# Performance work log

Hardware: AMD Instinct MI355X
Metric: run time of the kernel (lower is better)

The kernel has to match this reference:

```python
import jax, jax.numpy as jnp
import numpy as np

NHEAD, TOKEN_DIM, HIDDEN, OUT_DIM = 4, 768, 256, 768
B, L = 16, 1024
EPS = 1e-5
SLOPE = 0.01  # default LeakyReLU negative_slope


def _layernorm(x, g, b):
    mu = jnp.mean(x, axis=-1, keepdims=True)
    var = jnp.var(x, axis=-1, keepdims=True)
    return (x - mu) * jax.lax.rsqrt(var + EPS) * g + b


def setup_inputs() -> dict:
    key = jax.random.key(0)
    ks = jax.random.split(key, 8)
    s = 0.02
    return {
        "token_embedding": jax.random.normal(ks[0], (B, L, TOKEN_DIM), jnp.float32),
        "W_fc": jax.random.normal(ks[1], (NHEAD, TOKEN_DIM, HIDDEN), jnp.float32) * s,
        "b_fc": jnp.zeros((NHEAD, HIDDEN), jnp.float32),
        "ln_g": jnp.ones((NHEAD, HIDDEN), jnp.float32),
        "ln_b": jnp.zeros((NHEAD, HIDDEN), jnp.float32),
        "a_w": jax.random.normal(ks[2], (NHEAD, 2 * HIDDEN), jnp.float32) * s,
        "a_b": jnp.zeros((NHEAD,), jnp.float32),
        "W_cat": jax.random.normal(ks[3], (NHEAD * HIDDEN, OUT_DIM), jnp.float32) * s,
        "b_cat": jnp.zeros((OUT_DIM,), jnp.float32),
        "lnO_g": jnp.ones((OUT_DIM,), jnp.float32),
        "lnO_b": jnp.zeros((OUT_DIM,), jnp.float32),
        "W_fcs": jax.random.normal(ks[4], (3, OUT_DIM, OUT_DIM), jnp.float32) * s,
        "b_fcs": jnp.zeros((3, OUT_DIM), jnp.float32),
    }


def reference(token_embedding, W_fc, b_fc, ln_g, ln_b, a_w, a_b,
              W_cat, b_cat, lnO_g, lnO_b, W_fcs, b_fcs):
    # per-head projection + layernorm: h [n, B, L, H]
    h = jnp.einsum('bld,ndh->nblh', token_embedding, W_fc) + b_fc[:, None, None, :]
    h = _layernorm(h, ln_g[:, None, None, :], ln_b[:, None, None, :])
    # attn_fc(concat[h_j, h_i]) decomposes linearly:
    # score[n,b,i,j] = a1 . h[n,b,j] + a2 . h[n,b,i] + bias
    s_row = jnp.einsum('nblh,nh->nbl', h, a_w[:, :HIDDEN])   # varies with j
    s_col = jnp.einsum('nblh,nh->nbl', h, a_w[:, HIDDEN:])   # varies with i
    e = s_col[:, :, :, None] + s_row[:, :, None, :] + a_b[:, None, None, None]
    e = jnp.where(e >= 0, e, SLOPE * e)  # LeakyReLU
    attn = jax.nn.softmax(e, axis=-1)    # softmax over j
    h_prime = jnp.einsum('nbij,nbjh->nbih', attn, h)  # [n, B, L, H]
    # concat heads on feature dim -> [B, L, n*H]
    concat_out = jnp.transpose(h_prime, (1, 2, 0, 3)).reshape(B, L, NHEAD * HIDDEN)
    sent = jnp.mean(concat_out, axis=1)  # [B, n*H]
    sent = sent @ W_cat + b_cat
    sent = _layernorm(sent, lnO_g, lnO_b)
    dims_out = [sent @ W_fcs[i] + b_fcs[i] for i in range(3)]
    return (dims_out[0], dims_out[1], dims_out[2], sent)
```

## Files before the change

kernel.cpp:

```cpp
#include <hip/hip_runtime.h>
#include <math.h>


#define NH   4
#define TD   768
#define HID  256
#define OD   768
#define BB   16
#define LL   1024
#define RTOT (BB*LL)

typedef __attribute__((ext_vector_type(8))) short bf16x8;
typedef __attribute__((ext_vector_type(4))) float f32x4;

__device__ __forceinline__ float lrelu(float x) { return fmaxf(x, 0.01f * x); }

__device__ __forceinline__ float waveReduceSum(float v) {
  #pragma unroll
  for (int m = 1; m < 64; m <<= 1) v += __shfl_xor(v, m, 64);
  return v;
}
__device__ __forceinline__ float waveReduceMax(float v) {
  #pragma unroll
  for (int m = 1; m < 64; m <<= 1) v = fmaxf(v, __shfl_xor(v, m, 64));
  return v;
}
__device__ __forceinline__ float red16(float v) {
  v += __shfl_xor(v, 1, 64); v += __shfl_xor(v, 2, 64);
  v += __shfl_xor(v, 4, 64); v += __shfl_xor(v, 8, 64);
  return v;
}

__device__ __forceinline__ unsigned short f2b(float f) {
  union { float f; unsigned u; } v; v.f = f;
  unsigned u = v.u;
  return (unsigned short)((u + 0x7fffu + ((u >> 16) & 1u)) >> 16);
}
__device__ __forceinline__ float b2f(unsigned short h) {
  union { unsigned u; float f; } v; v.u = ((unsigned)h) << 16;
  return v.f;
}

__device__ __forceinline__ void gll16(const void* g, void* l) {
  __builtin_amdgcn_global_load_lds(
      (const __attribute__((address_space(1))) unsigned int*)g,
      (__attribute__((address_space(3))) unsigned int*)l, 16, 0, 0);
}

__global__ __launch_bounds__(256) void kconv(const float* __restrict__ T,
                                             const float* __restrict__ Wfc,
                                             unsigned short* __restrict__ Tb,
                                             unsigned short* __restrict__ Wtb) {
  __shared__ float tile[64][65];
  const int t = threadIdx.x;
  if (blockIdx.x < 6144) {
    const size_t i = ((size_t)blockIdx.x * 256 + t) * 8;
    const float4 a = *(const float4*)(T + i);
    const float4 b = *(const float4*)(T + i + 4);
    bf16x8 o;
    o[0] = (short)f2b(a.x); o[1] = (short)f2b(a.y);
    o[2] = (short)f2b(a.z); o[3] = (short)f2b(a.w);
    o[4] = (short)f2b(b.x); o[5] = (short)f2b(b.y);
    o[6] = (short)f2b(b.z); o[7] = (short)f2b(b.w);
    *(bf16x8*)(Tb + i) = o;
  } else {
    const int b2 = blockIdx.x - 6144;
    const int ct = b2 & 3;
    const int kt = (b2 >> 2) % 12;
    const int n  = b2 / 48;
    #pragma unroll
    for (int i = 0; i < 16; ++i) {
      const int kl = i * 4 + (t >> 6), cl = t & 63;
      tile[kl][cl] =
          Wfc[(size_t)n * TD * HID + (size_t)(kt * 64 + kl) * HID + ct * 64 + cl];
    }
    __syncthreads();
    #pragma unroll
    for (int i = 0; i < 16; ++i) {
      const int cl = i * 4 + (t >> 6), kl = t & 63;
      Wtb[(size_t)n * HID * TD + (size_t)(ct * 64 + cl) * TD + kt * 64 + kl] =
          f2b(tile[kl][cl]);
    }
  }
}

__global__ __launch_bounds__(512) void k1_mfma(
    const unsigned short* __restrict__ Tb,
    const unsigned short* __restrict__ Wtb,
    const float* __restrict__ bfc, const float* __restrict__ lng,
    const float* __restrict__ lnb, const float* __restrict__ aw,
    unsigned short* __restrict__ hb,
    float* __restrict__ sR, float* __restrict__ sC)
{
  const int n    = blockIdx.x >> 6;
  const int mb   = blockIdx.x & 63;
  const int t    = threadIdx.x;
  const int lane = t & 63;
  const int wq   = __builtin_amdgcn_readfirstlane(t >> 6);
  const int wm   = wq >> 1;
  const int wn   = wq & 1;
  const int cl   = lane & 15;
  const int rg   = lane >> 4;
  const int row0 = mb * 256;

  __shared__ __align__(16) char smem[131072];

  f32x4 acc[4][8];
  #pragma unroll
  for (int mi = 0; mi < 4; ++mi)
    #pragma unroll
    for (int ni = 0; ni < 8; ++ni) acc[mi][ni] = (f32x4){0.f, 0.f, 0.f, 0.f};

  const char* Tg = (const char*)Tb;
  const char* Wg = (const char*)(Wtb + (size_t)n * HID * TD);

  #define STAGE(buf, k0)                                                       \
    do {                                                                       \
      char* base_ = smem + (buf) * 65536;                                      \
      _Pragma("unroll")                                                        \
      for (int i_ = 0; i_ < 4; ++i_) {                                         \
        const int off_ = i_ * 8192 + t * 16;                                   \
        const int r_ = off_ >> 7, kb_ = off_ & 127;                            \
        const int kbs_ = kb_ ^ ((r_ & 7) << 4);                                \
        gll16(Tg + ((size_t)(row0 + r_) * TD + (k0)) * 2 + kbs_, base_ + off_);\
      }                                                                        \
      _Pragma("unroll")                                                        \
      for (int i_ = 0; i_ < 4; ++i_) {                                         \
        const int off_ = i_ * 8192 + t * 16;                                   \
        const int c_ = off_ >> 7, kb_ = off_ & 127;                            \
        const int kbs_ = kb_ ^ ((c_ & 7) << 4);                                \
        gll16(Wg + ((size_t)c_ * TD + (k0)) * 2 + kbs_, base_ + 32768 + off_); \
      }                                                                        \
    } while (0)

  STAGE(0, 0);
  __syncthreads();
  int cur = 0;
  for (int kt = 0; kt < 12; ++kt) {
    if (kt < 11) STAGE(cur ^ 1, (kt + 1) * 64);
    const char* As = smem + cur * 65536;
    const char* Bs = As + 32768;
    #pragma unroll
    for (int ks = 0; ks < 64; ks += 32) {
      bf16x8 av[4], bv[8];
      const int kk2 = (ks + rg * 8) * 2;
      #pragma unroll
      for (int mi = 0; mi < 4; ++mi) {
        const int row = wm * 64 + mi * 16 + cl;
        av[mi] = *(const bf16x8*)(As + row * 128 + (kk2 ^ ((row & 7) << 4)));
      }
      #pragma unroll
      for (int ni = 0; ni < 8; ++ni) {
        const int row = wn * 128 + ni * 16 + cl;
        bv[ni] = *(const bf16x8*)(Bs + row * 128 + (kk2 ^ ((row & 7) << 4)));
      }
      #pragma unroll
      for (int mi = 0; mi < 4; ++mi)
        #pragma unroll
        for (int ni = 0; ni < 8; ++ni)
          acc[mi][ni] = __builtin_amdgcn_mfma_f32_16x16x32_bf16(
              av[mi], bv[ni], acc[mi][ni], 0, 0, 0);
    }
    __syncthreads();
    cur ^= 1;
  }
  #undef STAGE

  unsigned short* hs = (unsigned short*)smem;
  float* redS  = (float*)(smem + 36864);
  float* redS2 = (float*)(smem + 38912);
  float* redP  = (float*)(smem + 40960);
  float* redC  = (float*)(smem + 43008);

  float bfn[8], gvn[8], bvn[8], a1n[8], a2n[8];
  #pragma unroll
  for (int ni = 0; ni < 8; ++ni) {
    const int c = wn * 128 + ni * 16 + cl;
    bfn[ni] = bfc[n * HID + c];
    gvn[ni] = lng[n * HID + c];
    bvn[ni] = lnb[n * HID + c];
    a1n[ni] = aw[n * (2 * HID) + c];
    a2n[ni] = aw[n * (2 * HID) + HID + c];
  }

  #pragma unroll
  for (int mi = 0; mi < 4; ++mi) {
    #pragma unroll
    for (int r = 0; r < 4; ++r) {
      float s = 0.f, s2 = 0.f;
      #pragma unroll
      for (int ni = 0; ni < 8; ++ni) {
        const float x = acc[mi][ni][r] + bfn[ni];
        acc[mi][ni][r] = x;
        s += x; s2 += x * x;
      }
      s = red16(s); s2 = red16(s2);
      if (cl == 0) {
        const int row = wm * 64 + mi * 16 + rg * 4 + r;
        redS [row * 2 + wn] = s;
        redS2[row * 2 + wn] = s2;
      }
    }
  }
  __syncthreads();

  #pragma unroll
  for (int mi = 0; mi < 4; ++mi) {
    #pragma unroll
    for (int r = 0; r < 4; ++r) {
      const int row = wm * 64 + mi * 16 + rg * 4 + r;
      const float st  = redS [row * 2] + redS [row * 2 + 1];
      const float s2t = redS2[row * 2] + redS2[row * 2 + 1];
      const float mu  = st * (1.f / HID);
      const float var = s2t * (1.f / HID) - mu * mu;
      const float rs  = rsqrtf(var + 1e-5f);
      float pr = 0.f, pc = 0.f;
      #pragma unroll
      for (int ni = 0; ni < 8; ++ni) {
        const float hv = (acc[mi][ni][r] - mu) * rs * gvn[ni] + bvn[ni];
        acc[mi][ni][r] = hv;
        pr += hv * a1n[ni]; pc += hv * a2n[ni];
      }
      pr = red16(pr); pc = red16(pc);
      if (cl == 0) { redP[row * 2 + wn] = pr; redC[row * 2 + wn] = pc; }
    }
  }
  __syncthreads();
  if (t < 256) {
    sR[n * RTOT + row0 + t] = redP[t * 2] + redP[t * 2 + 1];
    sC[n * RTOT + row0 + t] = redC[t * 2] + redC[t * 2 + 1];
  }

  unsigned short* hgb = hb + ((size_t)n * RTOT + row0) * HID;
  #pragma unroll
  for (int c = 0; c < 4; ++c) {
    #pragma unroll
    for (int ni = 0; ni < 8; ++ni)
      #pragma unroll
      for (int r = 0; r < 4; ++r) {
        const int lr  = wm * 16 + rg * 4 + r;
        const int col = wn * 128 + ni * 16 + cl;
        hs[lr * 264 + col] = f2b(acc[c][ni][r]);
      }
    __syncthreads();
    #pragma unroll
    for (int i = 0; i < 4; ++i) {
      const int idx = i * 4096 + t * 8;
      const int lr = idx >> 8, cc = idx & 255;
      const int grow = (lr >> 4) * 64 + c * 16 + (lr & 15);
      *(bf16x8*)&hgb[(size_t)grow * HID + cc] = *(const bf16x8*)&hs[lr * 264 + cc];
    }
    __syncthreads();
  }
}

__global__ __launch_bounds__(256) void k2_lse(
    const float* __restrict__ sR, const float* __restrict__ sC,
    const float* __restrict__ ab, float* __restrict__ q)
{
  const int n  = blockIdx.x >> 7;
  const int b  = (blockIdx.x >> 3) & 15;
  const int ic = blockIdx.x & 7;
  const int t  = threadIdx.x;
  const int base = (n * BB + b) * LL;

  __shared__ float rl[LL];
  __shared__ float red[4];

  const float4 r4 = ((const float4*)(sR + base))[t];
  ((float4*)rl)[t] = r4;
  float tm = fmaxf(fmaxf(r4.x, r4.y), fmaxf(r4.z, r4.w));
  tm = waveReduceMax(tm);
  if ((t & 63) == 0) red[t >> 6] = tm;
  __syncthreads();
  const float rmax = fmaxf(fmaxf(red[0], red[1]), fmaxf(red[2], red[3]));

  const int i  = ic * 128 + (t >> 1);
  const int jh = t & 1;
  const float ci = sC[base + i] + ab[n];
  const float m = lrelu(ci + rmax);
  float z0 = 0.f, z1 = 0.f, z2 = 0.f, z3 = 0.f;
  #pragma unroll 4
  for (int j4 = jh * 128; j4 < jh * 128 + 128; ++j4) {
    const float4 rr = ((const float4*)rl)[j4];
    z0 += __expf(lrelu(ci + rr.x) - m);
    z1 += __expf(lrelu(ci + rr.y) - m);
    z2 += __expf(lrelu(ci + rr.z) - m);
    z3 += __expf(lrelu(ci + rr.w) - m);
  }
  float z = (z0 + z1) + (z2 + z3);
  z += __shfl_xor(z, 1, 64);
  if (!jh) q[base + i] = m + __logf(z);
}

__global__ __launch_bounds__(256) void k23_colw(
    const unsigned short* __restrict__ h, const float* __restrict__ sR,
    const float* __restrict__ sC, const float* __restrict__ ab,
    const float* __restrict__ q, float* __restrict__ partial)
{
  const int n  = blockIdx.x >> 7;
  const int b  = (blockIdx.x >> 3) & 15;
  const int jc = blockIdx.x & 7;
  const int t  = threadIdx.x;
  const int base = (n * BB + b) * LL;

  __shared__ float cls[LL];
  __shared__ float qls[LL];
  __shared__ float wl[128];
  __shared__ float red2[8][256];

  ((float4*)cls)[t] = ((const float4*)(sC + base))[t];
  ((float4*)qls)[t] = ((const float4*)(q + base))[t];
  __syncthreads();

  {
    const int j  = jc * 128 + (t >> 1);
    const int ih = t & 1;
    const float rj = sR[base + j] + ab[n];
    float z0 = 0.f, z1 = 0.f, z2 = 0.f, z3 = 0.f;
    #pragma unroll 4
    for (int i4 = ih * 128; i4 < ih * 128 + 128; ++i4) {
      const float4 cc = ((const float4*)cls)[i4];
      const float4 qq = ((const float4*)qls)[i4];
      z0 += __expf(lrelu(cc.x + rj) - qq.x);
      z1 += __expf(lrelu(cc.y + rj) - qq.y);
      z2 += __expf(lrelu(cc.z + rj) - qq.z);
      z3 += __expf(lrelu(cc.w + rj) - qq.w);
    }
    float z = (z0 + z1) + (z2 + z3);
    z += __shfl_xor(z, 1, 64);
    if (!ih) wl[t >> 1] = z * (1.f / LL);
  }
  __syncthreads();

  const int jl = t >> 5;
  const int cg = t & 31;
  const unsigned short* hp =
      h + ((size_t)n * RTOT + b * LL + jc * 128) * HID + cg * 8;
  float a0=0,a1=0,a2=0,a3=0,a4=0,a5=0,a6=0,a7=0;
  #pragma unroll 4
  for (int j = jl; j < 128; j += 8) {
    const bf16x8 v = *(const bf16x8*)(hp + (size_t)j * HID);
    const float w = wl[j];
    a0 = fmaf(w, b2f((unsigned short)v[0]), a0);
    a1 = fmaf(w, b2f((unsigned short)v[1]), a1);
    a2 = fmaf(w, b2f((unsigned short)v[2]), a2);
    a3 = fmaf(w, b2f((unsigned short)v[3]), a3);
    a4 = fmaf(w, b2f((unsigned short)v[4]), a4);
    a5 = fmaf(w, b2f((unsigned short)v[5]), a5);
    a6 = fmaf(w, b2f((unsigned short)v[6]), a6);
    a7 = fmaf(w, b2f((unsigned short)v[7]), a7);
  }
  red2[jl][cg*8+0]=a0; red2[jl][cg*8+1]=a1; red2[jl][cg*8+2]=a2; red2[jl][cg*8+3]=a3;
  red2[jl][cg*8+4]=a4; red2[jl][cg*8+5]=a5; red2[jl][cg*8+6]=a6; red2[jl][cg*8+7]=a7;
  __syncthreads();
  float s = 0.f;
  #pragma unroll
  for (int r = 0; r < 8; ++r) s += red2[r][t];
  partial[((n * BB + b) * 8 + jc) * 256 + t] = s;
}

__global__ __launch_bounds__(256) void k4_cat(
    const float* __restrict__ partial, const float* __restrict__ Wcat,
    float* __restrict__ pcat)
{
  const int kc = blockIdx.x / 3;
  const int oc = blockIdx.x % 3;
  const int t  = threadIdx.x;
  __shared__ float s[64][16];
  {
    const int kk = t >> 2, b4 = (t & 3) * 4;
    const int n = kc >> 2;
    const int c = (kc & 3) * 64 + kk;
    #pragma unroll
    for (int bi = 0; bi < 4; ++bi) {
      const int b = b4 + bi;
      const float* pb = partial + (size_t)((n * BB + b) * 8) * 256 + c;
      float v = 0.f;
      #pragma unroll
      for (int j = 0; j < 8; ++j) v += pb[j * 256];
      s[kk][b] = v;
    }
  }
  __syncthreads();
  const int o = oc * 256 + t;
  const float* W = Wcat + (size_t)(kc * 64) * OD + o;
  float acc[BB];
  #pragma unroll
  for (int b = 0; b < BB; ++b) acc[b] = 0.f;
  #pragma unroll 4
  for (int kk = 0; kk < 64; ++kk) {
    const float w = W[(size_t)kk * OD];
    const f32x4 s0 = *(const f32x4*)&s[kk][0];
    const f32x4 s1 = *(const f32x4*)&s[kk][4];
    const f32x4 s2 = *(const f32x4*)&s[kk][8];
    const f32x4 s3 = *(const f32x4*)&s[kk][12];
    acc[0]=fmaf(s0.x,w,acc[0]);  acc[1]=fmaf(s0.y,w,acc[1]);
    acc[2]=fmaf(s0.z,w,acc[2]);  acc[3]=fmaf(s0.w,w,acc[3]);
    acc[4]=fmaf(s1.x,w,acc[4]);  acc[5]=fmaf(s1.y,w,acc[5]);
    acc[6]=fmaf(s1.z,w,acc[6]);  acc[7]=fmaf(s1.w,w,acc[7]);
    acc[8]=fmaf(s2.x,w,acc[8]);  acc[9]=fmaf(s2.y,w,acc[9]);
    acc[10]=fmaf(s2.z,w,acc[10]); acc[11]=fmaf(s2.w,w,acc[11]);
    acc[12]=fmaf(s3.x,w,acc[12]); acc[13]=fmaf(s3.y,w,acc[13]);
    acc[14]=fmaf(s3.z,w,acc[14]); acc[15]=fmaf(s3.w,w,acc[15]);
  }
  float* P = pcat + (size_t)(kc * BB) * OD + o;
  #pragma unroll
  for (int b = 0; b < BB; ++b) P[(size_t)b * OD] = acc[b];
}

__global__ __launch_bounds__(256) void k4_ln(
    const float* __restrict__ pcat, const float* __restrict__ bcat,
    const float* __restrict__ g, const float* __restrict__ be,
    float* __restrict__ sent, float* __restrict__ out_sent)
{
  const int b = blockIdx.x;
  const int t = threadIdx.x;
  __shared__ float red[4][2];
  float x[3];
  #pragma unroll
  for (int i = 0; i < 3; ++i) {
    const int o = i * 256 + t;
    float v = bcat[o];
    #pragma unroll
    for (int kc = 0; kc < 16; ++kc) v += pcat[(size_t)(kc * BB + b) * OD + o];
    x[i] = v;
  }
  float s  = x[0] + x[1] + x[2];
  float s2 = x[0]*x[0] + x[1]*x[1] + x[2]*x[2];
  s = waveReduceSum(s); s2 = waveReduceSum(s2);
  if ((t & 63) == 0) { red[t >> 6][0] = s; red[t >> 6][1] = s2; }
  __syncthreads();
  s  = red[0][0] + red[1][0] + red[2][0] + red[3][0];
  s2 = red[0][1] + red[1][1] + red[2][1] + red[3][1];
  const float mu  = s * (1.f / OD);
  const float var = s2 * (1.f / OD) - mu * mu;
  const float rs  = rsqrtf(var + 1e-5f);
  #pragma unroll
  for (int i = 0; i < 3; ++i) {
    const int o = i * 256 + t;
    const float y = (x[i] - mu) * rs * g[o] + be[o];
    sent[b * OD + o]     = y;
    out_sent[b * OD + o] = y;
  }
}

__global__ __launch_bounds__(256) void k4_fcs(
    const float* __restrict__ sent, const float* __restrict__ Wfcs,
    float* __restrict__ pfcs)
{
  const int kc = blockIdx.x / 9;
  const int r  = blockIdx.x % 9;
  const int i  = r / 3, oc = r % 3;
  const int t  = threadIdx.x;
  __shared__ float s[64][16];
  {
    const int kk = t >> 2, b4 = (t & 3) * 4;
    #pragma unroll
    for (int bi = 0; bi < 4; ++bi)
      s[kk][b4 + bi] = sent[(b4 + bi) * OD + kc * 64 + kk];
  }
  __syncthreads();
  const int o = oc * 256 + t;
  const float* W = Wfcs + (size_t)i * OD * OD + (size_t)(kc * 64) * OD + o;
  float acc[BB];
  #pragma unroll
  for (int b = 0; b < BB; ++b) acc[b] = 0.f;
  #pragma unroll 4
  for (int kk = 0; kk < 64; ++kk) {
    const float w = W[(size_t)kk * OD];
    const f32x4 s0 = *(const f32x4*)&s[kk][0];
    const f32x4 s1 = *(const f32x4*)&s[kk][4];
    const f32x4 s2 = *(const f32x4*)&s[kk][8];
    const f32x4 s3 = *(const f32x4*)&s[kk][12];
    acc[0]=fmaf(s0.x,w,acc[0]);  acc[1]=fmaf(s0.y,w,acc[1]);
    acc[2]=fmaf(s0.z,w,acc[2]);  acc[3]=fmaf(s0.w,w,acc[3]);
    acc[4]=fmaf(s1.x,w,acc[4]);  acc[5]=fmaf(s1.y,w,acc[5]);
    acc[6]=fmaf(s1.z,w,acc[6]);  acc[7]=fmaf(s1.w,w,acc[7]);
    acc[8]=fmaf(s2.x,w,acc[8]);  acc[9]=fmaf(s2.y,w,acc[9]);
    acc[10]=fmaf(s2.z,w,acc[10]); acc[11]=fmaf(s2.w,w,acc[11]);
    acc[12]=fmaf(s3.x,w,acc[12]); acc[13]=fmaf(s3.y,w,acc[13]);
    acc[14]=fmaf(s3.z,w,acc[14]); acc[15]=fmaf(s3.w,w,acc[15]);
  }
  float* P = pfcs + (size_t)((kc * 3 + i) * BB) * OD + o;
  #pragma unroll
  for (int b = 0; b < BB; ++b) P[(size_t)b * OD] = acc[b];
}

__global__ __launch_bounds__(256) void k4_red(
    const float* __restrict__ pfcs, const float* __restrict__ bfcs,
    float* __restrict__ out)
{
  const int i = blockIdx.x >> 4;
  const int b = blockIdx.x & 15;
  const int t = threadIdx.x;
  #pragma unroll
  for (int oc = 0; oc < 3; ++oc) {
    const int o = oc * 256 + t;
    float v = bfcs[i * OD + o];
    #pragma unroll
    for (int kc = 0; kc < 12; ++kc)
      v += pfcs[(size_t)((kc * 3 + i) * BB + b) * OD + o];
    out[i * (BB * OD) + b * OD + o] = v;
  }
}

extern "C" void kernel_launch(void* const* d_in, const int* in_sizes, int n_in,
                              void* d_out, int out_size, void* d_ws, size_t ws_size,
                              hipStream_t stream)
{
  const float* T    = (const float*)d_in[0];
  const float* Wfc  = (const float*)d_in[1];
  const float* bfc  = (const float*)d_in[2];
  const float* lng  = (const float*)d_in[3];
  const float* lnb  = (const float*)d_in[4];
  const float* aw   = (const float*)d_in[5];
  const float* ab   = (const float*)d_in[6];
  const float* Wcat = (const float*)d_in[7];
  const float* bcat = (const float*)d_in[8];
  const float* lnOg = (const float*)d_in[9];
  const float* lnOb = (const float*)d_in[10];
  const float* Wfcs = (const float*)d_in[11];
  const float* bfcs = (const float*)d_in[12];
  float* out = (float*)d_out;

  char* W = (char*)d_ws;
  unsigned short* Tb  = (unsigned short*)W;
  unsigned short* Wtb = (unsigned short*)(W + 25165824);
  unsigned short* hb  = (unsigned short*)(W + 26738688);
  float* sR      = (float*)(W + 60293120);
  float* sC      = sR + NH * RTOT;
  float* q       = sC + NH * RTOT;
  float* partial = q + NH * RTOT;
  float* sent    = partial + NH * BB * 8 * 256;
  float* pcat    = sent + BB * OD;
  float* pfcs    = pcat + 16 * BB * OD;

  kconv   <<<dim3(6336), dim3(256), 0, stream>>>(T, Wfc, Tb, Wtb);
  k1_mfma <<<dim3(256),  dim3(512), 0, stream>>>(Tb, Wtb, bfc, lng, lnb, aw, hb, sR, sC);
  k2_lse  <<<dim3(512),  dim3(256), 0, stream>>>(sR, sC, ab, q);
  k23_colw<<<dim3(512),  dim3(256), 0, stream>>>(hb, sR, sC, ab, q, partial);
  k4_cat  <<<dim3(48),   dim3(256), 0, stream>>>(partial, Wcat, pcat);
  k4_ln   <<<dim3(16),   dim3(256), 0, stream>>>(pcat, bcat, lnOg, lnOb, sent, out + 3 * BB * OD);
  k4_fcs  <<<dim3(108),  dim3(256), 0, stream>>>(sent, Wfcs, pfcs);
  k4_red  <<<dim3(48),   dim3(256), 0, stream>>>(pfcs, bfcs, out);
}
```

Before: 109.8 us.

## Restructure k1 GEMM into a 4-slot K=32 pipeline with a 2x4 wave grid

The projection GEMM kernel moves from a double-buffered K=64 loop with __syncthreads to a four-slot ring of K=32 stages. Loads are issued two stages ahead, split into A and B halves placed between MFMA groups, and synchronised with manual vmcnt waits, raw barriers and setprio. The wave layout changes from 4x2 to 2x4, so each wave computes 128x64 instead of 64x128, and launch bounds request two blocks per CU. The aim is to hide global-to-LDS latency and raise occupancy, at the cost of more barriers per K step and a fragile hand-written wait schedule.

```diff
diff --git a/kernel.cpp b/kernel.cpp
--- a/kernel.cpp
+++ b/kernel.cpp
@@ -84,7 +84,7 @@
   }
 }
 
-__global__ __launch_bounds__(512) void k1_mfma(
+__global__ __launch_bounds__(512, 2) void k1_mfma(
     const unsigned short* __restrict__ Tb,
     const unsigned short* __restrict__ Wtb,
     const float* __restrict__ bfc, const float* __restrict__ lng,
@@ -97,85 +97,122 @@
   const int t    = threadIdx.x;
   const int lane = t & 63;
   const int wq   = __builtin_amdgcn_readfirstlane(t >> 6);
-  const int wm   = wq >> 1;
-  const int wn   = wq & 1;
+  const int wm   = wq >> 2;
+  const int wn   = wq & 3;
   const int cl   = lane & 15;
   const int rg   = lane >> 4;
   const int row0 = mb * 256;
 
   __shared__ __align__(16) char smem[131072];
 
-  f32x4 acc[4][8];
-  #pragma unroll
-  for (int mi = 0; mi < 4; ++mi)
-    #pragma unroll
-    for (int ni = 0; ni < 8; ++ni) acc[mi][ni] = (f32x4){0.f, 0.f, 0.f, 0.f};
+  f32x4 acc[8][4];
+  #pragma unroll
+  for (int mi = 0; mi < 8; ++mi)
+    #pragma unroll
+    for (int ni = 0; ni < 4; ++ni) acc[mi][ni] = (f32x4){0.f, 0.f, 0.f, 0.f};
 
   const char* Tg = (const char*)Tb;
   const char* Wg = (const char*)(Wtb + (size_t)n * HID * TD);
 
-  #define STAGE(buf, k0)                                                       \
+  #define STAGE_A(slot, k0)                                                    \
     do {                                                                       \
-      char* base_ = smem + (buf) * 65536;                                      \
+      char* base_ = smem + (slot) * 32768;                                     \
       _Pragma("unroll")                                                        \
-      for (int i_ = 0; i_ < 4; ++i_) {                                         \
+      for (int i_ = 0; i_ < 2; ++i_) {                                         \
         const int off_ = i_ * 8192 + t * 16;                                   \
-        const int r_ = off_ >> 7, kb_ = off_ & 127;                            \
-        const int kbs_ = kb_ ^ ((r_ & 7) << 4);                                \
+        const int r_ = off_ >> 6, kb_ = off_ & 63;                             \
+        const int kbs_ = kb_ ^ ((r_ & 3) << 4);                                \
         gll16(Tg + ((size_t)(row0 + r_) * TD + (k0)) * 2 + kbs_, base_ + off_);\
       }                                                                        \
+    } while (0)
+  #define STAGE_B(slot, k0)                                                    \
+    do {                                                                       \
+      char* base_ = smem + (slot) * 32768 + 16384;                             \
       _Pragma("unroll")                                                        \
-      for (int i_ = 0; i_ < 4; ++i_) {                                         \
+      for (int i_ = 0; i_ < 2; ++i_) {                                         \
         const int off_ = i_ * 8192 + t * 16;                                   \
-        const int c_ = off_ >> 7, kb_ = off_ & 127;                            \
-        const int kbs_ = kb_ ^ ((c_ & 7) << 4);                                \
-        gll16(Wg + ((size_t)c_ * TD + (k0)) * 2 + kbs_, base_ + 32768 + off_); \
+        const int c_ = off_ >> 6, kb_ = off_ & 63;                             \
+        const int kbs_ = kb_ ^ ((c_ & 3) << 4);                                \
+        gll16(Wg + ((size_t)c_ * TD + (k0)) * 2 + kbs_, base_ + off_);         \
       }                                                                        \
     } while (0)
 
-  STAGE(0, 0);
-  __syncthreads();
-  int cur = 0;
-  for (int kt = 0; kt < 12; ++kt) {
-    if (kt < 11) STAGE(cur ^ 1, (kt + 1) * 64);
-    const char* As = smem + cur * 65536;
-    const char* Bs = As + 32768;
-    #pragma unroll
-    for (int ks = 0; ks < 64; ks += 32) {
-      bf16x8 av[4], bv[8];
-      const int kk2 = (ks + rg * 8) * 2;
+  STAGE_A(0, 0);  STAGE_B(0, 0);
+  STAGE_A(1, 32); STAGE_B(1, 32);
+
+  const int kk2 = rg * 16;
+
+  #pragma unroll 4
+  for (int kt = 0; kt < 24; ++kt) {
+    const int slot = kt & 3;
+    if (kt < 23) asm volatile("s_waitcnt vmcnt(4)" ::: "memory");
+    else         asm volatile("s_waitcnt vmcnt(0)" ::: "memory");
+    asm volatile("s_barrier" ::: "memory");
+
+    const char* As = smem + slot * 32768;
+    const char* Bs = As + 16384;
+
+    bf16x8 bv[4];
+    {
+      bf16x8 av[4];
       #pragma unroll
       for (int mi = 0; mi < 4; ++mi) {
-        const int row = wm * 64 + mi * 16 + cl;
-        av[mi] = *(const bf16x8*)(As + row * 128 + (kk2 ^ ((row & 7) << 4)));
-      }
-      #pragma unroll
-      for (int ni = 0; ni < 8; ++ni) {
-        const int row = wn * 128 + ni * 16 + cl;
-        bv[ni] = *(const bf16x8*)(Bs + row * 128 + (kk2 ^ ((row & 7) << 4)));
-      }
+        const int row = wm * 128 + mi * 16 + cl;
+        av[mi] = *(const bf16x8*)(As + row * 64 + (kk2 ^ ((row & 3) << 4)));
+      }
+      #pragma unroll
+      for (int ni = 0; ni < 4; ++ni) {
+        const int row = wn * 64 + ni * 16 + cl;
+        bv[ni] = *(const bf16x8*)(Bs + row * 64 + (kk2 ^ ((row & 3) << 4)));
+      }
+      if (kt < 22) STAGE_A((kt + 2) & 3, (kt + 2) * 32);
+      asm volatile("s_waitcnt lgkmcnt(0)" ::: "memory");
+      __builtin_amdgcn_sched_barrier(0);
+      __builtin_amdgcn_s_setprio(1);
       #pragma unroll
       for (int mi = 0; mi < 4; ++mi)
         #pragma unroll
-        for (int ni = 0; ni < 8; ++ni)
+        for (int ni = 0; ni < 4; ++ni)
           acc[mi][ni] = __builtin_amdgcn_mfma_f32_16x16x32_bf16(
               av[mi], bv[ni], acc[mi][ni], 0, 0, 0);
-    }
-    __syncthreads();
-    cur ^= 1;
-  }
-  #undef STAGE
-
-  unsigned short* hs = (unsigned short*)smem;
-  float* redS  = (float*)(smem + 36864);
-  float* redS2 = (float*)(smem + 38912);
-  float* redP  = (float*)(smem + 40960);
-  float* redC  = (float*)(smem + 43008);
-
-  float bfn[8], gvn[8], bvn[8], a1n[8], a2n[8];
-  #pragma unroll
-  for (int ni = 0; ni < 8; ++ni) {
-    const int c = wn * 128 + ni * 16 + cl;
+      __builtin_amdgcn_s_setprio(0);
+    }
+    asm volatile("s_barrier" ::: "memory");
+    {
+      bf16x8 av[4];
+      #pragma unroll
+      for (int mi = 0; mi < 4; ++mi) {
+        const int row = wm * 128 + (mi + 4) * 16 + cl;
+        av[mi] = *(const bf16x8*)(As + row * 64 + (kk2 ^ ((row & 3) << 4)));
+      }
+      if (kt < 22) STAGE_B((kt + 2) & 3, (kt + 2) * 32);
+      asm volatile("s_waitcnt lgkmcnt(0)" ::: "memory");
+      __builtin_amdgcn_sched_barrier(0);
+      __builtin_amdgcn_s_setprio(1);
+      #pragma unroll
+      for (int mi = 0; mi < 4; ++mi)
+        #pragma unroll
+        for (int ni = 0; ni < 4; ++ni)
+          acc[mi + 4][ni] = __builtin_amdgcn_mfma_f32_16x16x32_bf16(
+              av[mi], bv[ni], acc[mi + 4][ni], 0, 0, 0);
+      __builtin_amdgcn_s_setprio(0);
+    }
+  }
+  #undef STAGE_A
+  #undef STAGE_B
+
+  __syncthreads();
+
+  float* redS  = (float*)smem;
+  float* redS2 = (float*)(smem + 4096);
+  float* redP  = (float*)(smem + 8192);
+  float* redC  = (float*)(smem + 12288);
+  unsigned short* hs = (unsigned short*)(smem + 16384);
+
+  float bfn[4], gvn[4], bvn[4], a1n[4], a2n[4];
+  #pragma unroll
+  for (int ni = 0; ni < 4; ++ni) {
+    const int c = wn * 64 + ni * 16 + cl;
     bfn[ni] = bfc[n * HID + c];
     gvn[ni] = lng[n * HID + c];
     bvn[ni] = lnb[n * HID + c];
@@ -184,71 +221,76 @@
   }
 
   #pragma unroll
-  for (int mi = 0; mi < 4; ++mi) {
+  for (int mi = 0; mi < 8; ++mi) {
     #pragma unroll
     for (int r = 0; r < 4; ++r) {
       float s = 0.f, s2 = 0.f;
       #pragma unroll
-      for (int ni = 0; ni < 8; ++ni) {
+      for (int ni = 0; ni < 4; ++ni) {
         const float x = acc[mi][ni][r] + bfn[ni];
         acc[mi][ni][r] = x;
         s += x; s2 += x * x;
       }
       s = red16(s); s2 = red16(s2);
       if (cl == 0) {
-        const int row = wm * 64 + mi * 16 + rg * 4 + r;
-        redS [row * 2 + wn] = s;
-        redS2[row * 2 + wn] = s2;
-      }
-    }
-  }
-  __syncthreads();
-
-  #pragma unroll
-  for (int mi = 0; mi < 4; ++mi) {
+        const int lr = wm * 128 + mi * 16 + rg * 4 + r;
+        redS [lr * 4 + wn] = s;
+        redS2[lr * 4 + wn] = s2;
+      }
+    }
+  }
+  __syncthreads();
+
+  #pragma unroll
+  for (int mi = 0; mi < 8; ++mi) {
     #pragma unroll
     for (int r = 0; r < 4; ++r) {
-      const int row = wm * 64 + mi * 16 + rg * 4 + r;
-      const float st  = redS [row * 2] + redS [row * 2 + 1];
-      const float s2t = redS2[row * 2] + redS2[row * 2 + 1];
+      const int lr = wm * 128 + mi * 16 + rg * 4 + r;
+      const f32x4 sv  = *(const f32x4*)&redS [lr * 4];
+      const f32x4 s2v = *(const f32x4*)&redS2[lr * 4];
+      const float st  = sv.x + sv.y + sv.z + sv.w;
+      const float s2t = s2v.x + s2v.y + s2v.z + s2v.w;
       const float mu  = st * (1.f / HID);
       const float var = s2t * (1.f / HID) - mu * mu;
       const float rs  = rsqrtf(var + 1e-5f);
       float pr = 0.f, pc = 0.f;
       #pragma unroll
-      for (int ni = 0; ni < 8; ++ni) {
+      for (int ni = 0; ni < 4; ++ni) {
         const float hv = (acc[mi][ni][r] - mu) * rs * gvn[ni] + bvn[ni];
         acc[mi][ni][r] = hv;
         pr += hv * a1n[ni]; pc += hv * a2n[ni];
       }
       pr = red16(pr); pc = red16(pc);
-      if (cl == 0) { redP[row * 2 + wn] = pr; redC[row * 2 + wn] = pc; }
+      if (cl == 0) { redP[lr * 4 + wn] = pr; redC[lr * 4 + wn] = pc; }
     }
   }
   __syncthreads();
   if (t < 256) {
-    sR[n * RTOT + row0 + t] = redP[t * 2] + redP[t * 2 + 1];
-    sC[n * RTOT + row0 + t] = redC[t * 2] + redC[t * 2 + 1];
+    const f32x4 pv = *(const f32x4*)&redP[t * 4];
+    const f32x4 cv = *(const f32x4*)&redC[t * 4];
+    sR[n * RTOT + row0 + t] = pv.x + pv.y + pv.z + pv.w;
+    sC[n * RTOT + row0 + t] = cv.x + cv.y + cv.z + cv.w;
   }
 
   unsigned short* hgb = hb + ((size_t)n * RTOT + row0) * HID;
   #pragma unroll
-  for (int c = 0; c < 4; ++c) {
-    #pragma unroll
-    for (int ni = 0; ni < 8; ++ni)
+  for (int s = 0; s < 2; ++s) {
+    #pragma unroll
+    for (int mi = 0; mi < 4; ++mi)
       #pragma unroll
       for (int r = 0; r < 4; ++r) {
-        const int lr  = wm * 16 + rg * 4 + r;
-        const int col = wn * 128 + ni * 16 + cl;
-        hs[lr * 264 + col] = f2b(acc[c][ni][r]);
+        const int lr = wm * 64 + mi * 16 + rg * 4 + r;
+        #pragma unroll
+        for (int ni = 0; ni < 4; ++ni)
+          hs[lr * 264 + wn * 64 + ni * 16 + cl] = f2b(acc[s * 4 + mi][ni][r]);
       }
     __syncthreads();
     #pragma unroll
-    for (int i = 0; i < 4; ++i) {
-      const int idx = i * 4096 + t * 8;
-      const int lr = idx >> 8, cc = idx & 255;
-      const int grow = (lr >> 4) * 64 + c * 16 + (lr & 15);
-      *(bf16x8*)&hgb[(size_t)grow * HID + cc] = *(const bf16x8*)&hs[lr * 264 + cc];
+    for (int i = 0; i < 8; ++i) {
+      const int e  = i * 4096 + t * 8;
+      const int lr = e >> 8, cc = e & 255;
+      const int g  = (lr >> 6) * 128 + s * 64 + (lr & 63);
+      *(bf16x8*)&hgb[(size_t)g * HID + cc] = *(const bf16x8*)&hs[lr * 264 + cc];
     }
     __syncthreads();
   }
```

Result: slower. 118.4 us (+7.9%).

## Fuse fp32-to-bf16 token conversion into projection GEMM register-staged A loads

Applied to the files above, without the earlier changes.

Removes the separate pass that converted the whole token embedding to bf16. The GEMM now loads fp32 rows into registers, converts them in-kernel and writes them to swizzled LDS while the weights still go through direct global-to-LDS loads. Tiles shrink to 128 rows and K-steps of 32, with 256-thread blocks and two blocks per CU, doubling the grid. This saves a round trip over the large fp32 input and the bf16 copy, but it reads fp32 A once per head (four times) and adds register pressure and in-loop conversion work.

```diff
diff --git a/kernel.cpp b/kernel.cpp
--- a/kernel.cpp
+++ b/kernel.cpp
@@ -47,53 +47,38 @@
       (__attribute__((address_space(3))) unsigned int*)l, 16, 0, 0);
 }
 
-__global__ __launch_bounds__(256) void kconv(const float* __restrict__ T,
-                                             const float* __restrict__ Wfc,
-                                             unsigned short* __restrict__ Tb,
-                                             unsigned short* __restrict__ Wtb) {
+__global__ __launch_bounds__(256) void kconv_w(const float* __restrict__ src,
+                                               unsigned short* __restrict__ dst) {
   __shared__ float tile[64][65];
-  const int t = threadIdx.x;
-  if (blockIdx.x < 6144) {
-    const size_t i = ((size_t)blockIdx.x * 256 + t) * 8;
-    const float4 a = *(const float4*)(T + i);
-    const float4 b = *(const float4*)(T + i + 4);
-    bf16x8 o;
-    o[0] = (short)f2b(a.x); o[1] = (short)f2b(a.y);
-    o[2] = (short)f2b(a.z); o[3] = (short)f2b(a.w);
-    o[4] = (short)f2b(b.x); o[5] = (short)f2b(b.y);
-    o[6] = (short)f2b(b.z); o[7] = (short)f2b(b.w);
-    *(bf16x8*)(Tb + i) = o;
-  } else {
-    const int b2 = blockIdx.x - 6144;
-    const int ct = b2 & 3;
-    const int kt = (b2 >> 2) % 12;
-    const int n  = b2 / 48;
-    #pragma unroll
-    for (int i = 0; i < 16; ++i) {
-      const int kl = i * 4 + (t >> 6), cl = t & 63;
-      tile[kl][cl] =
-          Wfc[(size_t)n * TD * HID + (size_t)(kt * 64 + kl) * HID + ct * 64 + cl];
-    }
-    __syncthreads();
-    #pragma unroll
-    for (int i = 0; i < 16; ++i) {
-      const int cl = i * 4 + (t >> 6), kl = t & 63;
-      Wtb[(size_t)n * HID * TD + (size_t)(ct * 64 + cl) * TD + kt * 64 + kl] =
-          f2b(tile[kl][cl]);
-    }
-  }
-}
-
-__global__ __launch_bounds__(512) void k1_mfma(
-    const unsigned short* __restrict__ Tb,
+  const int t  = threadIdx.x;
+  const int ct = blockIdx.x & 3;
+  const int kt = (blockIdx.x >> 2) % 12;
+  const int n  = blockIdx.x / 48;
+  #pragma unroll
+  for (int i = 0; i < 16; ++i) {
+    const int kl = i * 4 + (t >> 6), cl = t & 63;
+    tile[kl][cl] =
+        src[(size_t)n * TD * HID + (size_t)(kt * 64 + kl) * HID + ct * 64 + cl];
+  }
+  __syncthreads();
+  #pragma unroll
+  for (int i = 0; i < 16; ++i) {
+    const int cl = i * 4 + (t >> 6), kl = t & 63;
+    dst[(size_t)n * HID * TD + (size_t)(ct * 64 + cl) * TD + kt * 64 + kl] =
+        f2b(tile[kl][cl]);
+  }
+}
+
+__global__ __launch_bounds__(256, 2) void k1_mfma(
+    const float* __restrict__ T,
     const unsigned short* __restrict__ Wtb,
     const float* __restrict__ bfc, const float* __restrict__ lng,
     const float* __restrict__ lnb, const float* __restrict__ aw,
     unsigned short* __restrict__ hb,
     float* __restrict__ sR, float* __restrict__ sC)
 {
-  const int n    = blockIdx.x >> 6;
-  const int mb   = blockIdx.x & 63;
+  const int n    = blockIdx.x >> 7;
+  const int mb   = blockIdx.x & 127;
   const int t    = threadIdx.x;
   const int lane = t & 63;
   const int wq   = __builtin_amdgcn_readfirstlane(t >> 6);
@@ -101,9 +86,9 @@
   const int wn   = wq & 1;
   const int cl   = lane & 15;
   const int rg   = lane >> 4;
-  const int row0 = mb * 256;
-
-  __shared__ __align__(16) char smem[131072];
+  const int row0 = mb * 128;
+
+  __shared__ __align__(16) char smem[49152];
 
   f32x4 acc[4][8];
   #pragma unroll
@@ -111,66 +96,103 @@
     #pragma unroll
     for (int ni = 0; ni < 8; ++ni) acc[mi][ni] = (f32x4){0.f, 0.f, 0.f, 0.f};
 
-  const char* Tg = (const char*)Tb;
   const char* Wg = (const char*)(Wtb + (size_t)n * HID * TD);
 
-  #define STAGE(buf, k0)                                                       \
+  #define LDA(r, k0)                                                           \
     do {                                                                       \
-      char* base_ = smem + (buf) * 65536;                                      \
+      _Pragma("unroll")                                                        \
+      for (int j_ = 0; j_ < 4; ++j_) {                                         \
+        const int row_ = j_ * 32 + (t >> 3);                                   \
+        r[j_] = *(const float4*)(T + (size_t)(row0 + row_) * TD + (k0) +       \
+                                 (t & 7) * 4);                                 \
+      }                                                                        \
+    } while (0)
+
+  #define WRA(slot, r)                                                         \
+    do {                                                                       \
+      char* ab_ = smem + (slot) * 24576;                                       \
+      _Pragma("unroll")                                                        \
+      for (int j_ = 0; j_ < 4; ++j_) {                                         \
+        const int row_ = j_ * 32 + (t >> 3);                                   \
+        const int byte_ = row_ * 64 + ((((t & 7) * 8)) ^ (((row_ >> 1) & 3) << 4)); \
+        uint2 p_;                                                              \
+        p_.x = (unsigned)f2b(r[j_].x) | ((unsigned)f2b(r[j_].y) << 16);        \
+        p_.y = (unsigned)f2b(r[j_].z) | ((unsigned)f2b(r[j_].w) << 16);        \
+        *(uint2*)(ab_ + byte_) = p_;                                           \
+      }                                                                        \
+    } while (0)
+
+  #define STAGE_B(slot, k0)                                                    \
+    do {                                                                       \
+      char* bb_ = smem + (slot) * 24576 + 8192;                                \
       _Pragma("unroll")                                                        \
       for (int i_ = 0; i_ < 4; ++i_) {                                         \
-        const int off_ = i_ * 8192 + t * 16;                                   \
-        const int r_ = off_ >> 7, kb_ = off_ & 127;                            \
-        const int kbs_ = kb_ ^ ((r_ & 7) << 4);                                \
-        gll16(Tg + ((size_t)(row0 + r_) * TD + (k0)) * 2 + kbs_, base_ + off_);\
+        const int off_ = i_ * 4096 + t * 16;                                   \
+        const int c_ = off_ >> 6, kb_ = off_ & 63;                             \
+        const int kbs_ = kb_ ^ (((c_ >> 1) & 3) << 4);                         \
+        gll16(Wg + ((size_t)c_ * TD + (k0)) * 2 + kbs_, bb_ + off_);           \
+      }                                                                        \
+    } while (0)
+
+  #define COMPUTE(slot)                                                        \
+    do {                                                                       \
+      const char* As_ = smem + (slot) * 24576;                                 \
+      const char* Bs_ = As_ + 8192;                                            \
+      bf16x8 av_[4], bv_[8];                                                   \
+      _Pragma("unroll")                                                        \
+      for (int mi = 0; mi < 4; ++mi) {                                         \
+        const int row_ = wm * 64 + mi * 16 + cl;                               \
+        av_[mi] = *(const bf16x8*)(As_ + row_ * 64 +                           \
+                                   ((rg * 16) ^ (((row_ >> 1) & 3) << 4)));    \
       }                                                                        \
       _Pragma("unroll")                                                        \
-      for (int i_ = 0; i_ < 4; ++i_) {                                         \
-        const int off_ = i_ * 8192 + t * 16;                                   \
-        const int c_ = off_ >> 7, kb_ = off_ & 127;                            \
-        const int kbs_ = kb_ ^ ((c_ & 7) << 4);                                \
-        gll16(Wg + ((size_t)c_ * TD + (k0)) * 2 + kbs_, base_ + 32768 + off_); \
+      for (int ni = 0; ni < 8; ++ni) {                                         \
+        const int row_ = wn * 128 + ni * 16 + cl;                              \
+        bv_[ni] = *(const bf16x8*)(Bs_ + row_ * 64 +                           \
+                                   ((rg * 16) ^ (((row_ >> 1) & 3) << 4)));    \
       }                                                                        \
+      _Pragma("unroll")                                                        \
+      for (int mi = 0; mi < 4; ++mi)                                           \
+        _Pragma("unroll")                                                      \
+        for (int ni = 0; ni < 8; ++ni)                                         \
+          acc[mi][ni] = __builtin_amdgcn_mfma_f32_16x16x32_bf16(               \
+              av_[mi], bv_[ni], acc[mi][ni], 0, 0, 0);                         \
     } while (0)
 
-  STAGE(0, 0);
-  __syncthreads();
-  int cur = 0;
-  for (int kt = 0; kt < 12; ++kt) {
-    if (kt < 11) STAGE(cur ^ 1, (kt + 1) * 64);
-    const char* As = smem + cur * 65536;
-    const char* Bs = As + 32768;
-    #pragma unroll
-    for (int ks = 0; ks < 64; ks += 32) {
-      bf16x8 av[4], bv[8];
-      const int kk2 = (ks + rg * 8) * 2;
-      #pragma unroll
-      for (int mi = 0; mi < 4; ++mi) {
-        const int row = wm * 64 + mi * 16 + cl;
-        av[mi] = *(const bf16x8*)(As + row * 128 + (kk2 ^ ((row & 7) << 4)));
-      }
-      #pragma unroll
-      for (int ni = 0; ni < 8; ++ni) {
-        const int row = wn * 128 + ni * 16 + cl;
-        bv[ni] = *(const bf16x8*)(Bs + row * 128 + (kk2 ^ ((row & 7) << 4)));
-      }
-      #pragma unroll
-      for (int mi = 0; mi < 4; ++mi)
-        #pragma unroll
-        for (int ni = 0; ni < 8; ++ni)
-          acc[mi][ni] = __builtin_amdgcn_mfma_f32_16x16x32_bf16(
-              av[mi], bv[ni], acc[mi][ni], 0, 0, 0);
-    }
-    __syncthreads();
-    cur ^= 1;
-  }
-  #undef STAGE
-
-  unsigned short* hs = (unsigned short*)smem;
-  float* redS  = (float*)(smem + 36864);
-  float* redS2 = (float*)(smem + 38912);
-  float* redP  = (float*)(smem + 40960);
-  float* redC  = (float*)(smem + 43008);
+  #define BODY(cur, rN, rF, kt)                                                \
+    do {                                                                       \
+      if ((kt) < 23) {                                                         \
+        WRA((cur) ^ 1, rN);                                                    \
+        STAGE_B((cur) ^ 1, ((kt) + 1) * 32);                                   \
+        if ((kt) < 22) LDA(rF, ((kt) + 2) * 32);                               \
+      }                                                                        \
+      COMPUTE(cur);                                                            \
+      __syncthreads();                                                         \
+    } while (0)
+
+  float4 rAa[4], rAb[4];
+  LDA(rAa, 0);
+  STAGE_B(0, 0);
+  LDA(rAb, 32);
+  WRA(0, rAa);
+  __syncthreads();
+
+  for (int kt2 = 0; kt2 < 12; ++kt2) {
+    const int kt = kt2 * 2;
+    BODY(0, rAb, rAa, kt);
+    BODY(1, rAa, rAb, kt + 1);
+  }
+  #undef LDA
+  #undef WRA
+  #undef STAGE_B
+  #undef COMPUTE
+  #undef BODY
+
+  float* redS  = (float*)smem;
+  float* redS2 = (float*)(smem + 1024);
+  float* redP  = (float*)(smem + 2048);
+  float* redC  = (float*)(smem + 3072);
+  unsigned short* hs = (unsigned short*)(smem + 4096);
 
   float bfn[8], gvn[8], bvn[8], a1n[8], a2n[8];
   #pragma unroll
@@ -196,9 +218,9 @@
       }
       s = red16(s); s2 = red16(s2);
       if (cl == 0) {
-        const int row = wm * 64 + mi * 16 + rg * 4 + r;
-        redS [row * 2 + wn] = s;
-        redS2[row * 2 + wn] = s2;
+        const int lr = wm * 64 + mi * 16 + rg * 4 + r;
+        redS [lr * 2 + wn] = s;
+        redS2[lr * 2 + wn] = s2;
       }
     }
   }
@@ -208,9 +230,9 @@
   for (int mi = 0; mi < 4; ++mi) {
     #pragma unroll
     for (int r = 0; r < 4; ++r) {
-      const int row = wm * 64 + mi * 16 + rg * 4 + r;
-      const float st  = redS [row * 2] + redS [row * 2 + 1];
-      const float s2t = redS2[row * 2] + redS2[row * 2 + 1];
+      const int lr = wm * 64 + mi * 16 + rg * 4 + r;
+      const float st  = redS [lr * 2] + redS [lr * 2 + 1];
+      const float s2t = redS2[lr * 2] + redS2[lr * 2 + 1];
       const float mu  = st * (1.f / HID);
       const float var = s2t * (1.f / HID) - mu * mu;
       const float rs  = rsqrtf(var + 1e-5f);
@@ -222,33 +244,36 @@
         pr += hv * a1n[ni]; pc += hv * a2n[ni];
       }
       pr = red16(pr); pc = red16(pc);
-      if (cl == 0) { redP[row * 2 + wn] = pr; redC[row * 2 + wn] = pc; }
+      if (cl == 0) { redP[lr * 2 + wn] = pr; redC[lr * 2 + wn] = pc; }
     }
   }
   __syncthreads();
-  if (t < 256) {
+  if (t < 128) {
     sR[n * RTOT + row0 + t] = redP[t * 2] + redP[t * 2 + 1];
     sC[n * RTOT + row0 + t] = redC[t * 2] + redC[t * 2 + 1];
   }
 
   unsigned short* hgb = hb + ((size_t)n * RTOT + row0) * HID;
   #pragma unroll
-  for (int c = 0; c < 4; ++c) {
-    #pragma unroll
-    for (int ni = 0; ni < 8; ++ni)
+  for (int s = 0; s < 2; ++s) {
+    if (wm == s) {
       #pragma unroll
-      for (int r = 0; r < 4; ++r) {
-        const int lr  = wm * 16 + rg * 4 + r;
-        const int col = wn * 128 + ni * 16 + cl;
-        hs[lr * 264 + col] = f2b(acc[c][ni][r]);
-      }
+      for (int mi = 0; mi < 4; ++mi)
+        #pragma unroll
+        for (int r = 0; r < 4; ++r) {
+          const int lr = mi * 16 + rg * 4 + r;
+          #pragma unroll
+          for (int ni = 0; ni < 8; ++ni)
+            hs[lr * 264 + wn * 128 + ni * 16 + cl] = f2b(acc[mi][ni][r]);
+        }
+    }
     __syncthreads();
     #pragma unroll
-    for (int i = 0; i < 4; ++i) {
-      const int idx = i * 4096 + t * 8;
-      const int lr = idx >> 8, cc = idx & 255;
-      const int grow = (lr >> 4) * 64 + c * 16 + (lr & 15);
-      *(bf16x8*)&hgb[(size_t)grow * HID + cc] = *(const bf16x8*)&hs[lr * 264 + cc];
+    for (int i = 0; i < 8; ++i) {
+      const int e  = i * 2048 + t * 8;
+      const int lr = e >> 8, cc = e & 255;
+      *(bf16x8*)&hgb[(size_t)(s * 64 + lr) * HID + cc] =
+          *(const bf16x8*)&hs[lr * 264 + cc];
     }
     __syncthreads();
   }
@@ -525,10 +550,9 @@
   float* out = (float*)d_out;
 
   char* W = (char*)d_ws;
-  unsigned short* Tb  = (unsigned short*)W;
-  unsigned short* Wtb = (unsigned short*)(W + 25165824);
-  unsigned short* hb  = (unsigned short*)(W + 26738688);
-  float* sR      = (float*)(W + 60293120);
+  unsigned short* Wtb = (unsigned short*)W;
+  unsigned short* hb  = (unsigned short*)(W + 1572864);
+  float* sR      = (float*)(W + 35127296);
   float* sC      = sR + NH * RTOT;
   float* q       = sC + NH * RTOT;
   float* partial = q + NH * RTOT;
@@ -536,8 +560,8 @@
   float* pcat    = sent + BB * OD;
   float* pfcs    = pcat + 16 * BB * OD;
 
-  kconv   <<<dim3(6336), dim3(256), 0, stream>>>(T, Wfc, Tb, Wtb);
-  k1_mfma <<<dim3(256),  dim3(512), 0, stream>>>(Tb, Wtb, bfc, lng, lnb, aw, hb, sR, sC);
+  kconv_w <<<dim3(192),  dim3(256), 0, stream>>>(Wfc, Wtb);
+  k1_mfma <<<dim3(512),  dim3(256), 0, stream>>>(T, Wtb, bfc, lng, lnb, aw, hb, sR, sC);
   k2_lse  <<<dim3(512),  dim3(256), 0, stream>>>(sR, sC, ab, q);
   k23_colw<<<dim3(512),  dim3(256), 0, stream>>>(hb, sR, sC, ab, q, partial);
   k4_cat  <<<dim3(48),   dim3(256), 0, stream>>>(partial, Wcat, pcat);
```

Result: slower. 112.7 us (+2.7%).
